# Kernel optimization log

Hardware: AMD Instinct MI355X
Metric: run time of the kernel (lower is better)

## Reference

```python
import jax, jax.numpy as jnp
import numpy as np

LN_EPS = 1e-5


def setup_inputs() -> dict:
    key = jax.random.key(0)
    k1, k2, k3, k4 = jax.random.split(key, 4)
    B, S, F, H = 128, 1024, 16, 512
    x = jax.random.normal(k1, (B, S, F), dtype=jnp.float32)
    # stacked per-feature Linear(1,H): W[i] = feature_projs[i].weight[:,0], b[i] = bias
    W = jax.random.normal(k2, (F, H), dtype=jnp.float32) * (1.0 / np.sqrt(F))
    b = jax.random.normal(k3, (F, H), dtype=jnp.float32) * 0.02
    emb = jax.random.normal(k4, (S, H), dtype=jnp.float32)  # num_stabilizers == S
    gamma = jnp.ones((H,), dtype=jnp.float32)
    beta = jnp.zeros((H,), dtype=jnp.float32)
    return {"x": x, "W": W, "b": b, "emb": emb, "gamma": gamma, "beta": beta}


def reference(x, W, b, emb, gamma, beta):
    # sum_i Linear_i(x[...,i:i+1]) == x @ W + sum_i b_i  (single fused GEMM)
    h = jnp.einsum("bsf,fh->bsh", x, W) + b.sum(axis=0)
    # index embedding: idx = arange(S), broadcast over batch
    h = h + emb[: x.shape[1]]  # (B,S,H) + (S,H)
    # LayerNorm over last dim
    mu = h.mean(axis=-1, keepdims=True)
    var = h.var(axis=-1, keepdims=True)
    hn = (h - mu) * jax.lax.rsqrt(var + LN_EPS)
    return hn * gamma + beta
```

## Files before the change

kernel.cpp:

```cpp
#include <hip/hip_runtime.h>

#define LN_EPS 1e-5f

static constexpr int Hc  = 512;
static constexpr int Fc  = 16;
static constexpr int Sc  = 1024;
static constexpr int NW  = 4096;

__global__ void bsum_kernel(const float* __restrict__ b, float* __restrict__ bsum) {
    int h = blockIdx.x * 64 + threadIdx.x;
    float s = 0.f;
#pragma unroll
    for (int i = 0; i < Fc; ++i) s += b[i * Hc + h];
    bsum[h] = s;
}

template <int CTRL, int RMASK>
__device__ __forceinline__ float dpp_add(float v) {
    int t = __builtin_amdgcn_update_dpp(0, __float_as_int(v), CTRL, RMASK, 0xf, true);
    return v + __int_as_float(t);
}
__device__ __forceinline__ float wave_sum64(float v) {
    v = dpp_add<0x111, 0xf>(v);
    v = dpp_add<0x112, 0xf>(v);
    v = dpp_add<0x114, 0xf>(v);
    v = dpp_add<0x118, 0xf>(v);
    v = dpp_add<0x142, 0xa>(v);
    v = dpp_add<0x143, 0xc>(v);
    return __int_as_float(__builtin_amdgcn_readlane(__float_as_int(v), 63));
}
__device__ __forceinline__ float rdlane(float v, int l) {
    return __int_as_float(__builtin_amdgcn_readlane(__float_as_int(v), l));
}

__device__ __forceinline__ unsigned rne16(float f) {
    unsigned u = __float_as_uint(f);
    return (u + 0x7fffu + ((u >> 16) & 1u)) >> 16;
}
__device__ __forceinline__ unsigned pack2(float lo, float hi) {
    return rne16(lo) | (rne16(hi) << 16);
}
__device__ __forceinline__ float lo_f(unsigned p) { return __uint_as_float(p << 16); }
__device__ __forceinline__ float hi_f(unsigned p) { return __uint_as_float(p); }

__global__ __launch_bounds__(256) void fused_kernel(
    const float* __restrict__ x, const float* __restrict__ W,
    const float* __restrict__ emb, const float* __restrict__ bsum,
    const float* __restrict__ gamma, const float* __restrict__ beta,
    float* __restrict__ out)
{
    const int lane = threadIdx.x & 63;
    const int w    = (blockIdx.x << 2) | (threadIdx.x >> 6);
    const int s    = w & (Sc - 1);
    const int h0 = lane * 4, h1 = h0 + 256;

    unsigned p00[Fc], p01[Fc], p10[Fc], p11[Fc];
#pragma unroll
    for (int i = 0; i < Fc; ++i) {
        const float4 wa = *reinterpret_cast<const float4*>(&W[i * Hc + h0]);
        const float4 wb = *reinterpret_cast<const float4*>(&W[i * Hc + h1]);
        p00[i] = pack2(wa.x, wa.y);
        p01[i] = pack2(wa.z, wa.w);
        p10[i] = pack2(wb.x, wb.y);
        p11[i] = pack2(wb.z, wb.w);
    }

    const int sub = lane >> 4, i16 = lane & 15;
    float xq[8];
#pragma unroll
    for (int q = 0; q < 8; ++q)
        xq[q] = __builtin_nontemporal_load(
            &x[((size_t)(q * 4 + sub) * NW + w) * Fc + i16]);

    const float4 g0  = *reinterpret_cast<const float4*>(&gamma[h0]);
    const float4 g1  = *reinterpret_cast<const float4*>(&gamma[h1]);
    const float4 be0 = *reinterpret_cast<const float4*>(&beta[h0]);
    const float4 be1 = *reinterpret_cast<const float4*>(&beta[h1]);
    float4 ebs0, ebs1;
    {
        const float4 e0  = *reinterpret_cast<const float4*>(&emb[(size_t)s * Hc + h0]);
        const float4 e1  = *reinterpret_cast<const float4*>(&emb[(size_t)s * Hc + h1]);
        const float4 bs0 = *reinterpret_cast<const float4*>(&bsum[h0]);
        const float4 bs1 = *reinterpret_cast<const float4*>(&bsum[h1]);
        ebs0.x = e0.x + bs0.x; ebs0.y = e0.y + bs0.y; ebs0.z = e0.z + bs0.z; ebs0.w = e0.w + bs0.w;
        ebs1.x = e1.x + bs1.x; ebs1.y = e1.y + bs1.y; ebs1.z = e1.z + bs1.z; ebs1.w = e1.w + bs1.w;
    }

    float4 rA0[4], rA1[4], rB0[4], rB1[4];

    auto BATCH = [&](int q, const float xsrc, float4* res0, float4* res1) {
#pragma unroll
        for (int u = 0; u < 4; ++u) {
            float4 a0 = ebs0, a1 = ebs1;
#pragma unroll
            for (int i = 0; i < Fc; ++i) {
                const float xi = rdlane(xsrc, u * 16 + i);
                a0.x = fmaf(xi, lo_f(p00[i]), a0.x);
                a0.y = fmaf(xi, hi_f(p00[i]), a0.y);
                a0.z = fmaf(xi, lo_f(p01[i]), a0.z);
                a0.w = fmaf(xi, hi_f(p01[i]), a0.w);
                a1.x = fmaf(xi, lo_f(p10[i]), a1.x);
                a1.y = fmaf(xi, hi_f(p10[i]), a1.y);
                a1.z = fmaf(xi, lo_f(p11[i]), a1.z);
                a1.w = fmaf(xi, hi_f(p11[i]), a1.w);
            }

            float psum = a0.x + a0.y + a0.z + a0.w + a1.x + a1.y + a1.z + a1.w;
            float pssq = fmaf(a0.x, a0.x, fmaf(a0.y, a0.y, fmaf(a0.z, a0.z, a0.w * a0.w)));
            pssq = fmaf(a1.x, a1.x, fmaf(a1.y, a1.y, fmaf(a1.z, a1.z, fmaf(a1.w, a1.w, pssq))));

            const float sum = wave_sum64(psum);
            const float ssq = wave_sum64(pssq);

            const float mean = sum * (1.0f / 512.0f);
            const float var  = ssq * (1.0f / 512.0f) - mean * mean;
            const float rs   = rsqrtf(var + LN_EPS);
            const float nmrs = -mean * rs;

            res0[u].x = fmaf(fmaf(a0.x, rs, nmrs), g0.x, be0.x);
            res0[u].y = fmaf(fmaf(a0.y, rs, nmrs), g0.y, be0.y);
            res0[u].z = fmaf(fmaf(a0.z, rs, nmrs), g0.z, be0.z);
            res0[u].w = fmaf(fmaf(a0.w, rs, nmrs), g0.w, be0.w);
            res1[u].x = fmaf(fmaf(a1.x, rs, nmrs), g1.x, be1.x);
            res1[u].y = fmaf(fmaf(a1.y, rs, nmrs), g1.y, be1.y);
            res1[u].z = fmaf(fmaf(a1.z, rs, nmrs), g1.z, be1.z);
            res1[u].w = fmaf(fmaf(a1.w, rs, nmrs), g1.w, be1.w);
        }
#pragma unroll
        for (int u = 0; u < 4; ++u) {
            float* orow = out + ((size_t)(q * 4 + u) * NW + w) * Hc;
            *reinterpret_cast<float4*>(&orow[h0]) = res0[u];
            *reinterpret_cast<float4*>(&orow[h1]) = res1[u];
        }
    };

#pragma unroll 1
    for (int qq = 0; qq < 4; ++qq) {
        BATCH(2 * qq,     xq[0], rA0, rA1);
        BATCH(2 * qq + 1, xq[1], rB0, rB1);
#pragma unroll
        for (int j = 0; j < 6; ++j) xq[j] = xq[j + 2];
    }
}

extern "C" void kernel_launch(void* const* d_in, const int* in_sizes, int n_in,
                              void* d_out, int out_size, void* d_ws, size_t ws_size,
                              hipStream_t stream) {
    const float* x     = (const float*)d_in[0];
    const float* W     = (const float*)d_in[1];
    const float* b     = (const float*)d_in[2];
    const float* emb   = (const float*)d_in[3];
    const float* gamma = (const float*)d_in[4];
    const float* beta  = (const float*)d_in[5];
    float* out  = (float*)d_out;
    float* bsum = (float*)d_ws;

    bsum_kernel<<<Hc / 64, 64, 0, stream>>>(b, bsum);

    const int blocks = NW / 4;
    fused_kernel<<<blocks, 256, 0, stream>>>(x, W, emb, bsum, gamma, beta, out);
}
```

Measured before the change: 59.88 us.

## Pack LayerNorm constants and results as fp16 pairs to cut register pressure

```diff
diff --git a/kernel.cpp b/kernel.cpp
--- a/kernel.cpp
+++ b/kernel.cpp
@@ -1,6 +1,8 @@
 #include <hip/hip_runtime.h>
 
 #define LN_EPS 1e-5f
+
+typedef __fp16 h2 __attribute__((ext_vector_type(2)));
 
 static constexpr int Hc  = 512;
 static constexpr int Fc  = 16;
@@ -43,7 +45,17 @@
 __device__ __forceinline__ float lo_f(unsigned p) { return __uint_as_float(p << 16); }
 __device__ __forceinline__ float hi_f(unsigned p) { return __uint_as_float(p); }
 
-__global__ __launch_bounds__(256) void fused_kernel(
+__device__ __forceinline__ unsigned pk16(float lo, float hi) {
+    return __builtin_bit_cast(unsigned, __builtin_amdgcn_cvt_pkrtz(lo, hi));
+}
+__device__ __forceinline__ float u16lo(unsigned p) {
+    h2 v = __builtin_bit_cast(h2, p); return (float)v.x;
+}
+__device__ __forceinline__ float u16hi(unsigned p) {
+    h2 v = __builtin_bit_cast(h2, p); return (float)v.y;
+}
+
+__global__ __launch_bounds__(256, 2) void fused_kernel(
     const float* __restrict__ x, const float* __restrict__ W,
     const float* __restrict__ emb, const float* __restrict__ bsum,
     const float* __restrict__ gamma, const float* __restrict__ beta,
@@ -72,42 +84,51 @@
         xq[q] = __builtin_nontemporal_load(
             &x[((size_t)(q * 4 + sub) * NW + w) * Fc + i16]);
 
-    const float4 g0  = *reinterpret_cast<const float4*>(&gamma[h0]);
-    const float4 g1  = *reinterpret_cast<const float4*>(&gamma[h1]);
-    const float4 be0 = *reinterpret_cast<const float4*>(&beta[h0]);
-    const float4 be1 = *reinterpret_cast<const float4*>(&beta[h1]);
-    float4 ebs0, ebs1;
+    unsigned e01, e23, e45, e67, gp01, gp23, gp45, gp67, bp01, bp23, bp45, bp67;
     {
         const float4 e0  = *reinterpret_cast<const float4*>(&emb[(size_t)s * Hc + h0]);
         const float4 e1  = *reinterpret_cast<const float4*>(&emb[(size_t)s * Hc + h1]);
         const float4 bs0 = *reinterpret_cast<const float4*>(&bsum[h0]);
         const float4 bs1 = *reinterpret_cast<const float4*>(&bsum[h1]);
-        ebs0.x = e0.x + bs0.x; ebs0.y = e0.y + bs0.y; ebs0.z = e0.z + bs0.z; ebs0.w = e0.w + bs0.w;
-        ebs1.x = e1.x + bs1.x; ebs1.y = e1.y + bs1.y; ebs1.z = e1.z + bs1.z; ebs1.w = e1.w + bs1.w;
+        e01 = pk16(e0.x + bs0.x, e0.y + bs0.y);
+        e23 = pk16(e0.z + bs0.z, e0.w + bs0.w);
+        e45 = pk16(e1.x + bs1.x, e1.y + bs1.y);
+        e67 = pk16(e1.z + bs1.z, e1.w + bs1.w);
+        const float4 g0  = *reinterpret_cast<const float4*>(&gamma[h0]);
+        const float4 g1  = *reinterpret_cast<const float4*>(&gamma[h1]);
+        const float4 be0 = *reinterpret_cast<const float4*>(&beta[h0]);
+        const float4 be1 = *reinterpret_cast<const float4*>(&beta[h1]);
+        gp01 = pk16(g0.x, g0.y); gp23 = pk16(g0.z, g0.w);
+        gp45 = pk16(g1.x, g1.y); gp67 = pk16(g1.z, g1.w);
+        bp01 = pk16(be0.x, be0.y); bp23 = pk16(be0.z, be0.w);
+        bp45 = pk16(be1.x, be1.y); bp67 = pk16(be1.z, be1.w);
     }
 
-    float4 rA0[4], rA1[4], rB0[4], rB1[4];
+    unsigned rA[16], rB[16];
 
-    auto BATCH = [&](int q, const float xsrc, float4* res0, float4* res1) {
+    auto BATCH = [&](int q, const float xsrc, unsigned* res) {
 #pragma unroll
         for (int u = 0; u < 4; ++u) {
-            float4 a0 = ebs0, a1 = ebs1;
+            float a0x = u16lo(e01), a0y = u16hi(e01);
+            float a0z = u16lo(e23), a0w = u16hi(e23);
+            float a1x = u16lo(e45), a1y = u16hi(e45);
+            float a1z = u16lo(e67), a1w = u16hi(e67);
 #pragma unroll
             for (int i = 0; i < Fc; ++i) {
                 const float xi = rdlane(xsrc, u * 16 + i);
-                a0.x = fmaf(xi, lo_f(p00[i]), a0.x);
-                a0.y = fmaf(xi, hi_f(p00[i]), a0.y);
-                a0.z = fmaf(xi, lo_f(p01[i]), a0.z);
-                a0.w = fmaf(xi, hi_f(p01[i]), a0.w);
-                a1.x = fmaf(xi, lo_f(p10[i]), a1.x);
-                a1.y = fmaf(xi, hi_f(p10[i]), a1.y);
-                a1.z = fmaf(xi, lo_f(p11[i]), a1.z);
-                a1.w = fmaf(xi, hi_f(p11[i]), a1.w);
+                a0x = fmaf(xi, lo_f(p00[i]), a0x);
+                a0y = fmaf(xi, hi_f(p00[i]), a0y);
+                a0z = fmaf(xi, lo_f(p01[i]), a0z);
+                a0w = fmaf(xi, hi_f(p01[i]), a0w);
+                a1x = fmaf(xi, lo_f(p10[i]), a1x);
+                a1y = fmaf(xi, hi_f(p10[i]), a1y);
+                a1z = fmaf(xi, lo_f(p11[i]), a1z);
+                a1w = fmaf(xi, hi_f(p11[i]), a1w);
             }
 
-            float psum = a0.x + a0.y + a0.z + a0.w + a1.x + a1.y + a1.z + a1.w;
-            float pssq = fmaf(a0.x, a0.x, fmaf(a0.y, a0.y, fmaf(a0.z, a0.z, a0.w * a0.w)));
-            pssq = fmaf(a1.x, a1.x, fmaf(a1.y, a1.y, fmaf(a1.z, a1.z, fmaf(a1.w, a1.w, pssq))));
+            float psum = a0x + a0y + a0z + a0w + a1x + a1y + a1z + a1w;
+            float pssq = fmaf(a0x, a0x, fmaf(a0y, a0y, fmaf(a0z, a0z, a0w * a0w)));
+            pssq = fmaf(a1x, a1x, fmaf(a1y, a1y, fmaf(a1z, a1z, fmaf(a1w, a1w, pssq))));
 
             const float sum = wave_sum64(psum);
             const float ssq = wave_sum64(pssq);
@@ -117,27 +138,37 @@
             const float rs   = rsqrtf(var + LN_EPS);
             const float nmrs = -mean * rs;
 
-            res0[u].x = fmaf(fmaf(a0.x, rs, nmrs), g0.x, be0.x);
-            res0[u].y = fmaf(fmaf(a0.y, rs, nmrs), g0.y, be0.y);
-            res0[u].z = fmaf(fmaf(a0.z, rs, nmrs), g0.z, be0.z);
-            res0[u].w = fmaf(fmaf(a0.w, rs, nmrs), g0.w, be0.w);
-            res1[u].x = fmaf(fmaf(a1.x, rs, nmrs), g1.x, be1.x);
-            res1[u].y = fmaf(fmaf(a1.y, rs, nmrs), g1.y, be1.y);
-            res1[u].z = fmaf(fmaf(a1.z, rs, nmrs), g1.z, be1.z);
-            res1[u].w = fmaf(fmaf(a1.w, rs, nmrs), g1.w, be1.w);
+            res[u * 4 + 0] = pk16(
+                fmaf(fmaf(a0x, rs, nmrs), u16lo(gp01), u16lo(bp01)),
+                fmaf(fmaf(a0y, rs, nmrs), u16hi(gp01), u16hi(bp01)));
+            res[u * 4 + 1] = pk16(
+                fmaf(fmaf(a0z, rs, nmrs), u16lo(gp23), u16lo(bp23)),
+                fmaf(fmaf(a0w, rs, nmrs), u16hi(gp23), u16hi(bp23)));
+            res[u * 4 + 2] = pk16(
+                fmaf(fmaf(a1x, rs, nmrs), u16lo(gp45), u16lo(bp45)),
+                fmaf(fmaf(a1y, rs, nmrs), u16hi(gp45), u16hi(bp45)));
+            res[u * 4 + 3] = pk16(
+                fmaf(fmaf(a1z, rs, nmrs), u16lo(gp67), u16lo(bp67)),
+                fmaf(fmaf(a1w, rs, nmrs), u16hi(gp67), u16hi(bp67)));
         }
+
 #pragma unroll
         for (int u = 0; u < 4; ++u) {
+            float4 r0, r1;
+            r0.x = u16lo(res[u * 4 + 0]); r0.y = u16hi(res[u * 4 + 0]);
+            r0.z = u16lo(res[u * 4 + 1]); r0.w = u16hi(res[u * 4 + 1]);
+            r1.x = u16lo(res[u * 4 + 2]); r1.y = u16hi(res[u * 4 + 2]);
+            r1.z = u16lo(res[u * 4 + 3]); r1.w = u16hi(res[u * 4 + 3]);
             float* orow = out + ((size_t)(q * 4 + u) * NW + w) * Hc;
-            *reinterpret_cast<float4*>(&orow[h0]) = res0[u];
-            *reinterpret_cast<float4*>(&orow[h1]) = res1[u];
+            *reinterpret_cast<float4*>(&orow[h0]) = r0;
+            *reinterpret_cast<float4*>(&orow[h1]) = r1;
         }
     };
 
 #pragma unroll 1
     for (int qq = 0; qq < 4; ++qq) {
-        BATCH(2 * qq,     xq[0], rA0, rA1);
-        BATCH(2 * qq + 1, xq[1], rB0, rB1);
+        BATCH(2 * qq,     xq[0], rA);
+        BATCH(2 * qq + 1, xq[1], rB);
 #pragma unroll
         for (int j = 0; j < 6; ++j) xq[j] = xq[j + 2];
     }
```

Result: slower. 75.19 us (+25.6%).
